# Optimization experiments

Hardware: AMD Instinct MI355X
Metric: run time of the kernel (lower is better)

## Reference

```python
import jax, jax.numpy as jnp
import numpy as np

NUM_CLASSES = 256
WEIGHT = 0.0005
EPS = 1e-12  # torch F.normalize eps


def setup_inputs() -> dict:
    key = jax.random.key(0)
    k1, k2 = jax.random.split(key)
    features = jax.random.normal(k1, (32768, 1024), dtype=jnp.float32)
    labels = jax.random.randint(k2, (32768,), 0, NUM_CLASSES, dtype=jnp.int32)
    return {"features": features, "labels": labels}


def _centroid_loss(features, labels):
    B, D = features.shape
    # row-wise L2 normalize (torch F.normalize: x / max(||x||, eps))
    norms = jnp.linalg.norm(features, axis=1, keepdims=True)
    f = features / jnp.maximum(norms, EPS)

    ones = jnp.ones((B,), f.dtype)
    counts = jax.ops.segment_sum(ones, labels, num_segments=NUM_CLASSES)  # [C]
    sums = jax.ops.segment_sum(f, labels, num_segments=NUM_CLASSES)       # [C, D]

    # rank of each sample within its class (order of first appearance),
    # matching the row order of features[class_mask] in the original loop
    onehot = jax.nn.one_hot(labels, NUM_CLASSES, dtype=jnp.int32)          # [B, C]
    rank = jnp.take_along_axis(jnp.cumsum(onehot, axis=0), labels[:, None].astype(jnp.int32), axis=1)[:, 0] - 1

    # idx_table[c, r] = global index of the r-th member of class c; sentinel B if none
    idx_table = jnp.full((NUM_CLASSES, B), B, dtype=jnp.int32)
    idx_table = idx_table.at[labels, rank].set(jnp.arange(B, dtype=jnp.int32))

    # NOTE: the original code indexes class_features with the GLOBAL index i
    # (arange(n_c) != i), i.e. it excludes the member of the class at position i,
    # and excludes nothing when i >= n_c. We reproduce that exactly.
    arange_b = jnp.arange(B)
    k = idx_table[labels, arange_b]            # class member at in-class position i (global i)
    valid_excl = k < B                          # exclusion only happens when i < class size
    excl_feat = jnp.where(valid_excl[:, None], f[jnp.where(valid_excl, k, 0)], 0.0)

    n_c = counts[labels]                        # class size per sample (float)
    denom = jnp.where(valid_excl, n_c - 1.0, n_c)
    denom = jnp.maximum(denom, 1.0)             # safe for masked-out singleton classes
    centroid = (sums[labels] - excl_feat) / denom[:, None]

    dist = jnp.mean((f - centroid) ** 2, axis=1)  # F.mse_loss(..., reduction='mean')
    contrib = jnp.where(n_c > 1.0, dist, 0.0)     # skip classes with <=1 sample
    return WEIGHT * jnp.sum(contrib) / B


def reference(features, labels):
    return _centroid_loss(features, labels)
```

## Files before the change

kernel.cpp:

```cpp
#include <hip/hip_runtime.h>

#define BN 32768
#define DN 1024
#define CN 256
#define RCAP 512
#define SUBS 8
#define WPB 4

__device__ __forceinline__ float dot4(float4 a, float4 b) {
    return a.x*b.x + a.y*b.y + a.z*b.z + a.w*b.w;
}

__global__ void __launch_bounds__(256) kc_compact(const int* __restrict__ labels,
                                                  int* __restrict__ idx,
                                                  int* __restrict__ counts) {
    __shared__ unsigned int packed[BN / 4];
    __shared__ int wcnt[4];
    const int c = blockIdx.x;
    const int t = threadIdx.x;

    for (int w = t; w < BN / 4; w += 256) {
        const int4 v = ((const int4*)labels)[w];
        packed[w] = (unsigned int)(v.x & 255)
                  | ((unsigned int)(v.y & 255) << 8)
                  | ((unsigned int)(v.z & 255) << 16)
                  | ((unsigned int)(v.w & 255) << 24);
    }
    __syncthreads();

    const int wave = t >> 6, lane = t & 63;
    const unsigned long long lt = (lane == 0) ? 0ull : (~0ull >> (64 - lane));
    const int ch0 = wave * 128, ch1 = ch0 + 128;

    int cnt = 0;
    for (int ch = ch0; ch < ch1; ++ch) {
        const int gi = ch * 64 + lane;
        const int lab = (packed[gi >> 2] >> ((gi & 3) * 8)) & 255;
        cnt += __popcll(__ballot(lab == c));
    }
    if (lane == 0) wcnt[wave] = cnt;
    __syncthreads();

    int base = 0;
    for (int w2 = 0; w2 < wave; ++w2) base += wcnt[w2];

    for (int ch = ch0; ch < ch1; ++ch) {
        const int gi = ch * 64 + lane;
        const int lab = (packed[gi >> 2] >> ((gi & 3) * 8)) & 255;
        const bool pred = (lab == c);
        const unsigned long long mask = __ballot(pred);
        if (pred) {
            const int pos = base + __popcll(mask & lt);
            if (pos < RCAP) idx[c * RCAP + pos] = gi;
        }
        base += __popcll(mask);
    }
    if (t == 0) counts[c] = wcnt[0] + wcnt[1] + wcnt[2] + wcnt[3];
}

__global__ void __launch_bounds__(256, 4) k_gather(const float4* __restrict__ x4,
                                                   const int* __restrict__ idx,
                                                   const int* __restrict__ counts,
                                                   float* __restrict__ rnorm,
                                                   float4* __restrict__ partials) {
    __shared__ float facc[(DN / 4) * 5];
    const int b = blockIdx.x;
    const int c = b >> 3;
    const int sub = b & 7;
    const int t = threadIdx.x;
    const int wave = t >> 6, lane = t & 63;
    const int ws = sub * WPB + wave;
    const int nn = min(counts[c], RCAP);

    for (int i = t; i < (DN / 4) * 5; i += 256) facc[i] = 0.0f;

    int myidx = 0;
    {
        const int r = ws + 32 * lane;
        if (lane < 16 && r < nn) myidx = idx[c * RCAP + r];
    }
    const int nrows = (nn > ws) ? ((nn - ws + 31) >> 5) : 0;

    float4 a0 = make_float4(0.f, 0.f, 0.f, 0.f), a1 = a0, a2 = a0, a3 = a0;

    if (nrows > 0) {
        int row = __shfl(myidx, 0, 64);
        const float4* rb = x4 + (size_t)row * 256;
        float4 v0 = rb[lane], v1 = rb[lane + 64], v2 = rb[lane + 128], v3 = rb[lane + 192];
        for (int j = 0; j < nrows; ++j) {
            int nrow = 0;
            float4 n0 = make_float4(0.f, 0.f, 0.f, 0.f), n1 = n0, n2 = n0, n3 = n0;
            if (j + 1 < nrows) {
                nrow = __shfl(myidx, j + 1, 64);
                const float4* nb = x4 + (size_t)nrow * 256;
                n0 = nb[lane]; n1 = nb[lane + 64]; n2 = nb[lane + 128]; n3 = nb[lane + 192];
            }
            float ss = dot4(v0, v0) + dot4(v1, v1) + dot4(v2, v2) + dot4(v3, v3);
#pragma unroll
            for (int off = 32; off; off >>= 1) ss += __shfl_xor(ss, off, 64);
            const float rn = 1.0f / fmaxf(sqrtf(ss), 1e-12f);
            if (lane == 0) rnorm[row] = rn;
            a0.x += v0.x * rn; a0.y += v0.y * rn; a0.z += v0.z * rn; a0.w += v0.w * rn;
            a1.x += v1.x * rn; a1.y += v1.y * rn; a1.z += v1.z * rn; a1.w += v1.w * rn;
            a2.x += v2.x * rn; a2.y += v2.y * rn; a2.z += v2.z * rn; a2.w += v2.w * rn;
            a3.x += v3.x * rn; a3.y += v3.y * rn; a3.z += v3.z * rn; a3.w += v3.w * rn;
            row = nrow; v0 = n0; v1 = n1; v2 = n2; v3 = n3;
        }
    }

    __syncthreads();
    {
        const int q0 = lane, q1 = lane + 64, q2 = lane + 128, q3 = lane + 192;
        atomicAdd(&facc[5 * q0 + 0], a0.x); atomicAdd(&facc[5 * q0 + 1], a0.y);
        atomicAdd(&facc[5 * q0 + 2], a0.z); atomicAdd(&facc[5 * q0 + 3], a0.w);
        atomicAdd(&facc[5 * q1 + 0], a1.x); atomicAdd(&facc[5 * q1 + 1], a1.y);
        atomicAdd(&facc[5 * q1 + 2], a1.z); atomicAdd(&facc[5 * q1 + 3], a1.w);
        atomicAdd(&facc[5 * q2 + 0], a2.x); atomicAdd(&facc[5 * q2 + 1], a2.y);
        atomicAdd(&facc[5 * q2 + 2], a2.z); atomicAdd(&facc[5 * q2 + 3], a2.w);
        atomicAdd(&facc[5 * q3 + 0], a3.x); atomicAdd(&facc[5 * q3 + 1], a3.y);
        atomicAdd(&facc[5 * q3 + 2], a3.z); atomicAdd(&facc[5 * q3 + 3], a3.w);
    }
    __syncthreads();

    const float4 tot = make_float4(facc[5 * t + 0], facc[5 * t + 1],
                                   facc[5 * t + 2], facc[5 * t + 3]);
    partials[(size_t)b * 256 + t] = tot;
}

__global__ void __launch_bounds__(256) k_red(const float4* __restrict__ partials,
                                             const int* __restrict__ counts,
                                             float* __restrict__ sums,
                                             float* __restrict__ snorm2,
                                             float* __restrict__ acc) {
    __shared__ float wred[4];
    const int c = blockIdx.x;
    const int t = threadIdx.x;
    const int wave = t >> 6, lane = t & 63;

    float4 tot = make_float4(0.f, 0.f, 0.f, 0.f);
#pragma unroll
    for (int s = 0; s < SUBS; ++s) {
        const float4 p = partials[(size_t)(c * SUBS + s) * 256 + t];
        tot.x += p.x; tot.y += p.y; tot.z += p.z; tot.w += p.w;
    }
    ((float4*)sums)[(size_t)c * 256 + t] = tot;

    float d = dot4(tot, tot);
#pragma unroll
    for (int off = 32; off; off >>= 1) d += __shfl_xor(d, off, 64);
    if (lane == 0) wred[wave] = d;
    __syncthreads();
    if (t == 0) {
        const float s2 = wred[0] + wred[1] + wred[2] + wred[3];
        snorm2[c] = s2;
        const int n = counts[c];
        if (n > 1) {
            const float nf = (float)n;
            atomicAdd(acc, (nf - s2 / nf) * (1.0f / DN));
        }
    }
}

__global__ void __launch_bounds__(256) k_corr(const float4* __restrict__ x4,
                                              const int* __restrict__ labels,
                                              const int* __restrict__ counts,
                                              const int* __restrict__ idx,
                                              const float* __restrict__ rnorm,
                                              const float* __restrict__ sums,
                                              const float* __restrict__ snorm2,
                                              float* __restrict__ acc) {
    const int i = blockIdx.x;
    const int c = labels[i];
    const int n = counts[c];
    if (i >= n || n < 2 || i >= RCAP) return;
    const int k = idx[c * RCAP + i];
    const int t = threadIdx.x;

    const float4 xi = x4[(size_t)i * 256 + t];
    const float4 xk = x4[(size_t)k * 256 + t];
    const float4 s  = ((const float4*)sums)[(size_t)c * 256 + t];

    float d0 = dot4(xi, s);
    float d1 = dot4(xi, xk);
    float d2 = dot4(xk, s);
    float d3 = dot4(xk, xk);
#pragma unroll
    for (int off = 32; off; off >>= 1) {
        d0 += __shfl_xor(d0, off, 64);
        d1 += __shfl_xor(d1, off, 64);
        d2 += __shfl_xor(d2, off, 64);
        d3 += __shfl_xor(d3, off, 64);
    }
    __shared__ float4 wred[4];
    if ((t & 63) == 0) wred[t >> 6] = make_float4(d0, d1, d2, d3);
    __syncthreads();
    if (t == 0) {
        const float xiS  = wred[0].x + wred[1].x + wred[2].x + wred[3].x;
        const float xixk = wred[0].y + wred[1].y + wred[2].y + wred[3].y;
        const float xkS  = wred[0].z + wred[1].z + wred[2].z + wred[3].z;
        const float xkxk = wred[0].w + wred[1].w + wred[2].w + wred[3].w;
        const float rni = rnorm[i], rnk = rnorm[k], s2 = snorm2[c];
        const float fiS  = rni * xiS;
        const float fifk = rni * rnk * xixk;
        const float Sfk  = rnk * xkS;
        const float fk2  = rnk * rnk * xkxk;
        const float nf = (float)n;
        const float dd = nf - 1.0f;
        const float naive = -2.0f * fiS / nf + s2 / (nf * nf);
        const float corr  = -2.0f * (fiS - fifk) / dd + (s2 - 2.0f * Sfk + fk2) / (dd * dd);
        atomicAdd(acc, (corr - naive) * (1.0f / DN));
    }
}

__global__ void k_fin(const float* __restrict__ acc, float* __restrict__ out) {
    out[0] = (0.0005f / (float)BN) * acc[0];
}

extern "C" void kernel_launch(void* const* d_in, const int* in_sizes, int n_in,
                              void* d_out, int out_size, void* d_ws, size_t ws_size,
                              hipStream_t stream) {
    const float* features = (const float*)d_in[0];
    const int* labels = (const int*)d_in[1];
    float* out = (float*)d_out;

    char* ws = (char*)d_ws;
    float4* partials = (float4*)(ws + 0);
    float*  rnorm    = (float*)(ws + 8388608);
    float*  sums     = (float*)(ws + 8519680);
    int*    idx      = (int*)  (ws + 9568256);
    int*    counts   = (int*)  (ws + 10092544);
    float*  snorm2   = (float*)(ws + 10093568);
    float*  acc      = (float*)(ws + 10094592);

    const float4* x4 = (const float4*)features;

    hipMemsetAsync(acc, 0, sizeof(float), stream);
    kc_compact<<<CN, 256, 0, stream>>>(labels, idx, counts);
    k_gather<<<CN * SUBS, 256, 0, stream>>>(x4, idx, counts, rnorm, partials);
    k_red<<<CN, 256, 0, stream>>>(partials, counts, sums, snorm2, acc);
    k_corr<<<RCAP, 256, 0, stream>>>(x4, labels, counts, idx, rnorm, sums, snorm2, acc);
    k_fin<<<1, 1, 0, stream>>>(acc, out);
}
```

Baseline: 255.4 us.

## Split row-norm into separate pass and restructure class gather to block-per-row

Row inverse norms now come from a dedicated streaming kernel, one wave per row. The gather kernel then only accumulates pre-scaled rows. In the gather, each block stages its class's row indices and norms in shared memory, and each thread loads four rows at a time across all 256 float4 columns. This removes the per-wave shuffle reduction and the shared-memory atomic merge. The cost is reading the full feature matrix twice (once for norms, once for gathering), in exchange for more memory-level parallelism in the gather.

```diff
diff --git a/kernel.cpp b/kernel.cpp
--- a/kernel.cpp
+++ b/kernel.cpp
@@ -5,7 +5,6 @@
 #define CN 256
 #define RCAP 512
 #define SUBS 8
-#define WPB 4
 
 __device__ __forceinline__ float dot4(float4 a, float4 b) {
     return a.x*b.x + a.y*b.y + a.z*b.z + a.w*b.w;
@@ -58,73 +57,61 @@
     if (t == 0) counts[c] = wcnt[0] + wcnt[1] + wcnt[2] + wcnt[3];
 }
 
-__global__ void __launch_bounds__(256, 4) k_gather(const float4* __restrict__ x4,
-                                                   const int* __restrict__ idx,
-                                                   const int* __restrict__ counts,
-                                                   float* __restrict__ rnorm,
-                                                   float4* __restrict__ partials) {
-    __shared__ float facc[(DN / 4) * 5];
+__global__ void __launch_bounds__(256) k_rnorm(const float4* __restrict__ x4,
+                                               float* __restrict__ rnorm) {
+    const int wave = threadIdx.x >> 6;
+    const int lane = threadIdx.x & 63;
+    const int row = blockIdx.x * 4 + wave;
+    const float4* base = x4 + (size_t)row * (DN / 4);
+    const float4 v0 = base[lane];
+    const float4 v1 = base[lane + 64];
+    const float4 v2 = base[lane + 128];
+    const float4 v3 = base[lane + 192];
+    float ss = dot4(v0, v0) + dot4(v1, v1) + dot4(v2, v2) + dot4(v3, v3);
+#pragma unroll
+    for (int off = 32; off; off >>= 1) ss += __shfl_xor(ss, off, 64);
+    if (lane == 0) rnorm[row] = 1.0f / fmaxf(sqrtf(ss), 1e-12f);
+}
+
+__global__ void __launch_bounds__(256) k_gather2(const float4* __restrict__ x4,
+                                                 const int* __restrict__ idx,
+                                                 const int* __restrict__ counts,
+                                                 const float* __restrict__ rnorm,
+                                                 float4* __restrict__ partials) {
+    __shared__ int sic[RCAP];
+    __shared__ float srn[RCAP];
     const int b = blockIdx.x;
     const int c = b >> 3;
     const int sub = b & 7;
     const int t = threadIdx.x;
-    const int wave = t >> 6, lane = t & 63;
-    const int ws = sub * WPB + wave;
+
     const int nn = min(counts[c], RCAP);
-
-    for (int i = t; i < (DN / 4) * 5; i += 256) facc[i] = 0.0f;
-
-    int myidx = 0;
-    {
-        const int r = ws + 32 * lane;
-        if (lane < 16 && r < nn) myidx = idx[c * RCAP + r];
-    }
-    const int nrows = (nn > ws) ? ((nn - ws + 31) >> 5) : 0;
-
-    float4 a0 = make_float4(0.f, 0.f, 0.f, 0.f), a1 = a0, a2 = a0, a3 = a0;
-
-    if (nrows > 0) {
-        int row = __shfl(myidx, 0, 64);
-        const float4* rb = x4 + (size_t)row * 256;
-        float4 v0 = rb[lane], v1 = rb[lane + 64], v2 = rb[lane + 128], v3 = rb[lane + 192];
-        for (int j = 0; j < nrows; ++j) {
-            int nrow = 0;
-            float4 n0 = make_float4(0.f, 0.f, 0.f, 0.f), n1 = n0, n2 = n0, n3 = n0;
-            if (j + 1 < nrows) {
-                nrow = __shfl(myidx, j + 1, 64);
-                const float4* nb = x4 + (size_t)nrow * 256;
-                n0 = nb[lane]; n1 = nb[lane + 64]; n2 = nb[lane + 128]; n3 = nb[lane + 192];
-            }
-            float ss = dot4(v0, v0) + dot4(v1, v1) + dot4(v2, v2) + dot4(v3, v3);
-#pragma unroll
-            for (int off = 32; off; off >>= 1) ss += __shfl_xor(ss, off, 64);
-            const float rn = 1.0f / fmaxf(sqrtf(ss), 1e-12f);
-            if (lane == 0) rnorm[row] = rn;
-            a0.x += v0.x * rn; a0.y += v0.y * rn; a0.z += v0.z * rn; a0.w += v0.w * rn;
-            a1.x += v1.x * rn; a1.y += v1.y * rn; a1.z += v1.z * rn; a1.w += v1.w * rn;
-            a2.x += v2.x * rn; a2.y += v2.y * rn; a2.z += v2.z * rn; a2.w += v2.w * rn;
-            a3.x += v3.x * rn; a3.y += v3.y * rn; a3.z += v3.z * rn; a3.w += v3.w * rn;
-            row = nrow; v0 = n0; v1 = n1; v2 = n2; v3 = n3;
-        }
-    }
-
-    __syncthreads();
-    {
-        const int q0 = lane, q1 = lane + 64, q2 = lane + 128, q3 = lane + 192;
-        atomicAdd(&facc[5 * q0 + 0], a0.x); atomicAdd(&facc[5 * q0 + 1], a0.y);
-        atomicAdd(&facc[5 * q0 + 2], a0.z); atomicAdd(&facc[5 * q0 + 3], a0.w);
-        atomicAdd(&facc[5 * q1 + 0], a1.x); atomicAdd(&facc[5 * q1 + 1], a1.y);
-        atomicAdd(&facc[5 * q1 + 2], a1.z); atomicAdd(&facc[5 * q1 + 3], a1.w);
-        atomicAdd(&facc[5 * q2 + 0], a2.x); atomicAdd(&facc[5 * q2 + 1], a2.y);
-        atomicAdd(&facc[5 * q2 + 2], a2.z); atomicAdd(&facc[5 * q2 + 3], a2.w);
-        atomicAdd(&facc[5 * q3 + 0], a3.x); atomicAdd(&facc[5 * q3 + 1], a3.y);
-        atomicAdd(&facc[5 * q3 + 2], a3.z); atomicAdd(&facc[5 * q3 + 3], a3.w);
-    }
-    __syncthreads();
-
-    const float4 tot = make_float4(facc[5 * t + 0], facc[5 * t + 1],
-                                   facc[5 * t + 2], facc[5 * t + 3]);
-    partials[(size_t)b * 256 + t] = tot;
+    const int nnpad = min((nn + 31) & ~31, RCAP);
+
+    for (int i = t; i < nnpad; i += 256) {
+        const int r = min(i, nn - 1);
+        const int row = idx[c * RCAP + r];
+        sic[i] = row;
+        srn[i] = (i < nn) ? rnorm[row] : 0.0f;
+    }
+    __syncthreads();
+
+    float4 acc = make_float4(0.f, 0.f, 0.f, 0.f);
+    for (int base = sub * 4; base < nnpad; base += 32) {
+        const int row0 = sic[base + 0], row1 = sic[base + 1];
+        const int row2 = sic[base + 2], row3 = sic[base + 3];
+        const float rn0 = srn[base + 0], rn1 = srn[base + 1];
+        const float rn2 = srn[base + 2], rn3 = srn[base + 3];
+        const float4 v0 = x4[(size_t)row0 * 256 + t];
+        const float4 v1 = x4[(size_t)row1 * 256 + t];
+        const float4 v2 = x4[(size_t)row2 * 256 + t];
+        const float4 v3 = x4[(size_t)row3 * 256 + t];
+        acc.x += v0.x * rn0; acc.y += v0.y * rn0; acc.z += v0.z * rn0; acc.w += v0.w * rn0;
+        acc.x += v1.x * rn1; acc.y += v1.y * rn1; acc.z += v1.z * rn1; acc.w += v1.w * rn1;
+        acc.x += v2.x * rn2; acc.y += v2.y * rn2; acc.z += v2.z * rn2; acc.w += v2.w * rn2;
+        acc.x += v3.x * rn3; acc.y += v3.y * rn3; acc.z += v3.z * rn3; acc.w += v3.w * rn3;
+    }
+    partials[(size_t)b * 256 + t] = acc;
 }
 
 __global__ void __launch_bounds__(256) k_red(const float4* __restrict__ partials,
@@ -236,7 +223,8 @@
 
     hipMemsetAsync(acc, 0, sizeof(float), stream);
     kc_compact<<<CN, 256, 0, stream>>>(labels, idx, counts);
-    k_gather<<<CN * SUBS, 256, 0, stream>>>(x4, idx, counts, rnorm, partials);
+    k_rnorm<<<BN / 4, 256, 0, stream>>>(x4, rnorm);
+    k_gather2<<<CN * SUBS, 256, 0, stream>>>(x4, idx, counts, rnorm, partials);
     k_red<<<CN, 256, 0, stream>>>(partials, counts, sums, snorm2, acc);
     k_corr<<<RCAP, 256, 0, stream>>>(x4, labels, counts, idx, rnorm, sums, snorm2, acc);
     k_fin<<<1, 1, 0, stream>>>(acc, out);
```

Result: faster. 239.7 us (-6.1%).
